# Kernel tuning notes

Hardware: AMD Instinct MI355X
Metric: run time of the kernel (lower is better)

Reference implementation:

```python
import jax, jax.numpy as jnp
import numpy as np

EPS = 1e-8
NUM_ITERATIONS = 3


def layer_norm(x, g, b, eps=EPS):
    m = jnp.mean(x, axis=-1, keepdims=True)
    v = jnp.mean((x - m) ** 2, axis=-1, keepdims=True)
    return (x - m) * jax.lax.rsqrt(v + eps) * g + b


def gru_cell(x, h, w_ih, w_hh, b_ih, b_hh):
    # PyTorch GRUCell: gates ordered (r, z, n)
    gi = x @ w_ih.T + b_ih  # [B*S, 3D]
    gh = h @ w_hh.T + b_hh
    i_r, i_z, i_n = jnp.split(gi, 3, axis=-1)
    h_r, h_z, h_n = jnp.split(gh, 3, axis=-1)
    r = jax.nn.sigmoid(i_r + h_r)
    z = jax.nn.sigmoid(i_z + h_z)
    n = jnp.tanh(i_n + r * h_n)
    return (1.0 - z) * n + z * h


def setup_inputs() -> dict:
    key = jax.random.key(0)
    ks = jax.random.split(key, 12)
    B, N, D, S = 64, 1024, 512, 16
    s = 1.0 / np.sqrt(D)
    return {
        "inputs": jax.random.normal(ks[0], (B, N, D), jnp.float32),
        "noise": jax.random.normal(ks[1], (B, S, D), jnp.float32),
        "slot_mu": jax.random.normal(ks[2], (1, 1, D), jnp.float32),
        "slot_log_sigma": jnp.zeros((1, 1, D), jnp.float32),
        "ln_in_g": jnp.ones((D,), jnp.float32),
        "ln_in_b": jnp.zeros((D,), jnp.float32),
        "ln_slots_g": jnp.ones((D,), jnp.float32),
        "ln_slots_b": jnp.zeros((D,), jnp.float32),
        "ln_mlp_g": jnp.ones((D,), jnp.float32),
        "ln_mlp_b": jnp.zeros((D,), jnp.float32),
        "Wq": jax.random.normal(ks[3], (D, D), jnp.float32) * s,
        "Wk": jax.random.normal(ks[4], (D, D), jnp.float32) * s,
        "Wv": jax.random.normal(ks[5], (D, D), jnp.float32) * s,
        "gru_w_ih": jax.random.normal(ks[6], (3 * D, D), jnp.float32) * s,
        "gru_w_hh": jax.random.normal(ks[7], (3 * D, D), jnp.float32) * s,
        "gru_b_ih": jnp.zeros((3 * D,), jnp.float32),
        "gru_b_hh": jnp.zeros((3 * D,), jnp.float32),
        "mlp_w1": jax.random.normal(ks[8], (D, D), jnp.float32) * s,
        "mlp_b1": jnp.zeros((D,), jnp.float32),
        "mlp_w2": jax.random.normal(ks[9], (D, D), jnp.float32) * s,
        "mlp_b2": jnp.zeros((D,), jnp.float32),
    }


def reference(inputs, noise, slot_mu, slot_log_sigma,
              ln_in_g, ln_in_b, ln_slots_g, ln_slots_b, ln_mlp_g, ln_mlp_b,
              Wq, Wk, Wv, gru_w_ih, gru_w_hh, gru_b_ih, gru_b_hh,
              mlp_w1, mlp_b1, mlp_w2, mlp_b2):
    B, N, D = inputs.shape
    S = noise.shape[1]
    scale = D ** (-0.5)

    # slot init: mu + sigma * eps
    slots = slot_mu + jnp.exp(slot_log_sigma) * noise  # [B,S,D]

    x = layer_norm(inputs, ln_in_g, ln_in_b)
    k = x @ Wk.T  # [B,N,D]
    v = x @ Wv.T

    for _ in range(NUM_ITERATIONS):
        slots_prev = slots
        sn = layer_norm(slots, ln_slots_g, ln_slots_b)
        q = sn @ Wq.T  # [B,S,D]
        attn_logits = jnp.einsum("bnd,bmd->bnm", q, k) * scale  # [B,S,N]
        attn = jax.nn.softmax(attn_logits, axis=-1)
        attn = attn / (jnp.sum(attn, axis=1, keepdims=True) + EPS)  # column-normalize over slots
        updates = jnp.einsum("bnm,bmd->bnd", attn, v)  # [B,S,D]
        slots = gru_cell(updates.reshape(-1, D), slots_prev.reshape(-1, D),
                         gru_w_ih, gru_w_hh, gru_b_ih, gru_b_hh).reshape(B, S, D)
        h = jax.nn.relu(layer_norm(slots, ln_mlp_g, ln_mlp_b) @ mlp_w1.T + mlp_b1)
        slots = slots + h @ mlp_w2.T + mlp_b2

    # proj_to_hidden is Identity (slot_dim == hidden_size); forward_dtype=float32
    return slots
```

## Files before the change

kernel.cpp:

```cpp
#include <hip/hip_runtime.h>
#include <hip/hip_bf16.h>
#include <cstdint>
#include <cstddef>


typedef __bf16 bf16x8 __attribute__((ext_vector_type(8)));
typedef float f32x4 __attribute__((ext_vector_type(4)));

__device__ __forceinline__ float bf2f(unsigned int u) {
  union { unsigned int i; float f; } v; v.i = u << 16; return v.f;
}
__device__ __forceinline__ unsigned short f2bf(float x) {
  __hip_bfloat16 h = __float2bfloat16(x);
  unsigned short u;
  __builtin_memcpy(&u, &h, 2);
  return u;
}

#define GLD16(gp, lp)                                                       \
  __builtin_amdgcn_global_load_lds(                                         \
      (const __attribute__((address_space(1))) void*)(gp),                  \
      (__attribute__((address_space(3))) void*)(lp), 16, 0, 0)


__global__ void wprep_k(const float* __restrict__ Wv, const float* __restrict__ w1,
                        const float* __restrict__ w2, const float* __restrict__ wih,
                        const float* __restrict__ whh, const float* __restrict__ bih,
                        const float* __restrict__ bhh, const float* __restrict__ mu,
                        const float* __restrict__ ls, const float* __restrict__ noise,
                        unsigned short* __restrict__ wv_bf, unsigned short* __restrict__ w1_bf,
                        unsigned short* __restrict__ w2_bf, unsigned short* __restrict__ wcat,
                        float* __restrict__ bcat, float* __restrict__ slots) {
  int blk = blockIdx.x, t = threadIdx.x;
  if (blk < 1024) {
    int i = blk * 256 + t; wv_bf[i] = f2bf(Wv[i]);
  } else if (blk < 2048) {
    int i = (blk - 1024) * 256 + t; w1_bf[i] = f2bf(w1[i]);
  } else if (blk < 3072) {
    int i = (blk - 2048) * 256 + t; w2_bf[i] = f2bf(w2[i]);
  } else if (blk < 11264) {
    int i = (blk - 3072) * 256 + t;
    int j = i >> 10, k = i & 1023;
    float v;
    if (j < 1024)      v = (k < 512) ? wih[j * 512 + k] : whh[j * 512 + (k - 512)];
    else if (j < 1536) v = (k < 512) ? wih[j * 512 + k] : 0.0f;
    else               v = (k < 512) ? 0.0f : whh[(j - 512) * 512 + (k - 512)];
    wcat[i] = f2bf(v);
  } else if (blk < 11272) {
    int j = (blk - 11264) * 256 + t;
    float v;
    if (j < 1024)      v = bih[j] + bhh[j];
    else if (j < 1536) v = bih[j];
    else               v = bhh[j - 512];
    bcat[j] = v;
  } else {
    int i = (blk - 11272) * 256 + t;
    int d = i & 511;
    slots[i] = mu[d] + expf(ls[d]) * noise[i];
  }
}

__global__ __launch_bounds__(256) void tcast2_k(const float* __restrict__ Wq,
                                                const float* __restrict__ Wk,
                                                unsigned short* __restrict__ wqT,
                                                unsigned short* __restrict__ wkT) {
  __shared__ float tt[32][33];
  const float* in = blockIdx.z ? Wk : Wq;
  unsigned short* out = blockIdx.z ? wkT : wqT;
  int c0 = blockIdx.x << 5, r0 = blockIdx.y << 5;
  int tx = threadIdx.x & 31, ty = threadIdx.x >> 5;
  #pragma unroll
  for (int i = 0; i < 4; ++i)
    tt[ty + 8 * i][tx] = in[(size_t)(r0 + ty + 8 * i) * 512 + c0 + tx];
  __syncthreads();
  #pragma unroll
  for (int i = 0; i < 4; ++i)
    out[(size_t)(c0 + ty + 8 * i) * 512 + r0 + tx] = f2bf(tt[tx][ty + 8 * i]);
}


__global__ __launch_bounds__(256) void ln_rows_k(
    const float* __restrict__ in, const float* __restrict__ g, const float* __restrict__ b,
    unsigned short* __restrict__ out, int rows) {
  int w = threadIdx.x >> 6, lane = threadIdx.x & 63;
  int row = (blockIdx.x << 2) + w;
  if (row >= rows) return;
  const float4* rp = reinterpret_cast<const float4*>(in + (size_t)row * 512);
  float4 v0 = rp[lane], v1 = rp[lane + 64];
  float s = v0.x + v0.y + v0.z + v0.w + v1.x + v1.y + v1.z + v1.w;
  float q = v0.x*v0.x + v0.y*v0.y + v0.z*v0.z + v0.w*v0.w
          + v1.x*v1.x + v1.y*v1.y + v1.z*v1.z + v1.w*v1.w;
  #pragma unroll
  for (int o = 32; o > 0; o >>= 1) { s += __shfl_xor(s, o); q += __shfl_xor(q, o); }
  float m = s * (1.0f / 512.0f);
  float rstd = rsqrtf(q * (1.0f / 512.0f) - m * m + 1e-8f);
  const float4* gp = reinterpret_cast<const float4*>(g);
  const float4* bp = reinterpret_cast<const float4*>(b);
  float4 g0 = gp[lane], g1 = gp[lane + 64];
  float4 b0 = bp[lane], b1 = bp[lane + 64];
  ushort4 o0, o1;
  o0.x = f2bf((v0.x - m) * rstd * g0.x + b0.x);
  o0.y = f2bf((v0.y - m) * rstd * g0.y + b0.y);
  o0.z = f2bf((v0.z - m) * rstd * g0.z + b0.z);
  o0.w = f2bf((v0.w - m) * rstd * g0.w + b0.w);
  o1.x = f2bf((v1.x - m) * rstd * g1.x + b1.x);
  o1.y = f2bf((v1.y - m) * rstd * g1.y + b1.y);
  o1.z = f2bf((v1.z - m) * rstd * g1.z + b1.z);
  o1.w = f2bf((v1.w - m) * rstd * g1.w + b1.w);
  ushort4* op = reinterpret_cast<ushort4*>(out + (size_t)row * 512);
  op[lane] = o0; op[lane + 64] = o1;
}

__global__ __launch_bounds__(256) void gru_ln_k(
    const float* __restrict__ gates, const float* __restrict__ hp,
    const float* __restrict__ g, const float* __restrict__ b,
    float* __restrict__ sgru, unsigned short* __restrict__ lnm) {
  int w = threadIdx.x >> 6, lane = threadIdx.x & 63;
  int row = (blockIdx.x << 2) + w;
  size_t gb = (size_t)row * 2048 + (lane << 3);
  size_t hb = (size_t)row * 512 + (lane << 3);
  float rs[8], zs[8], in_[8], hn[8], hv[8], y[8];
  #pragma unroll
  for (int c = 0; c < 2; ++c) {
    *reinterpret_cast<float4*>(rs + 4*c)  = *reinterpret_cast<const float4*>(gates + gb + 4*c);
    *reinterpret_cast<float4*>(zs + 4*c)  = *reinterpret_cast<const float4*>(gates + gb + 512 + 4*c);
    *reinterpret_cast<float4*>(in_ + 4*c) = *reinterpret_cast<const float4*>(gates + gb + 1024 + 4*c);
    *reinterpret_cast<float4*>(hn + 4*c)  = *reinterpret_cast<const float4*>(gates + gb + 1536 + 4*c);
    *reinterpret_cast<float4*>(hv + 4*c)  = *reinterpret_cast<const float4*>(hp + hb + 4*c);
  }
  float s = 0.f, q = 0.f;
  #pragma unroll
  for (int j = 0; j < 8; ++j) {
    float r = 1.0f / (1.0f + expf(-rs[j]));
    float z = 1.0f / (1.0f + expf(-zs[j]));
    float n = tanhf(in_[j] + r * hn[j]);
    float h = (1.0f - z) * n + z * hv[j];
    y[j] = h; s += h; q += h * h;
  }
  #pragma unroll
  for (int o = 32; o > 0; o >>= 1) { s += __shfl_xor(s, o); q += __shfl_xor(q, o); }
  float m = s * (1.0f / 512.0f);
  float rstd = rsqrtf(q * (1.0f / 512.0f) - m * m + 1e-8f);
  const float* gg = g + (lane << 3);
  const float* bb = b + (lane << 3);
  #pragma unroll
  for (int c = 0; c < 2; ++c)
    *reinterpret_cast<float4*>(sgru + hb + 4*c) = *reinterpret_cast<const float4*>(y + 4*c);
  uint4 o4;
  unsigned int p[8];
  #pragma unroll
  for (int j = 0; j < 8; ++j) p[j] = f2bf((y[j] - m) * rstd * gg[j] + bb[j]);
  o4.x = p[0] | (p[1] << 16); o4.y = p[2] | (p[3] << 16);
  o4.z = p[4] | (p[5] << 16); o4.w = p[6] | (p[7] << 16);
  *reinterpret_cast<uint4*>(lnm + hb) = o4;
}


__global__ __launch_bounds__(256) void gemm_vt(
    const unsigned short* __restrict__ A, const unsigned short* __restrict__ W,
    unsigned short* __restrict__ vT) {
  __shared__ unsigned short sA[2][4096];
  __shared__ unsigned short sB[2][4096];
  const int tid = threadIdx.x;
  const int lane = tid & 63, w = tid >> 6;

  int flat = blockIdx.y * 4 + blockIdx.x;
  { int c = 2048 >> 3; flat = (flat & 7) * c + (flat >> 3); }
  const int row0 = (flat >> 2) << 7;
  const int col0 = (flat & 3) << 7;
  const int K = 512;

  const int wm = (w >> 1) << 6, wn = (w & 1) << 6;
  const int lrow = lane & 15, kt = (lane >> 4) << 3;
  const int srow = lane >> 2, scol = (lane & 3) << 3;

  f32x4 acc[4][4];
  #pragma unroll
  for (int m = 0; m < 4; ++m)
    #pragma unroll
    for (int n = 0; n < 4; ++n) acc[m][n] = f32x4{0.f, 0.f, 0.f, 0.f};

  auto stage = [&](int buf, int k0) {
    #pragma unroll
    for (int i = 0; i < 2; ++i) {
      int ii = w * 2 + i;
      int r = (ii << 4) + srow;
      GLD16(A + (size_t)(row0 + r) * K + k0 + scol, &sA[buf][ii * 512]);
      GLD16(W + (size_t)(col0 + r) * K + k0 + scol, &sB[buf][ii * 512]);
    }
  };

  stage(0, 0);
  int cur = 0;
  for (int t = 0; t < 16; ++t) {
    __syncthreads();
    if (t + 1 < 16) stage(cur ^ 1, (t + 1) << 5);
    bf16x8 af[4], bfv[4];
    #pragma unroll
    for (int m = 0; m < 4; ++m)
      af[m] = *reinterpret_cast<const bf16x8*>(&sA[cur][(wm + m * 16 + lrow) * 32 + kt]);
    #pragma unroll
    for (int n = 0; n < 4; ++n)
      bfv[n] = *reinterpret_cast<const bf16x8*>(&sB[cur][(wn + n * 16 + lrow) * 32 + kt]);
    #pragma unroll
    for (int m = 0; m < 4; ++m)
      #pragma unroll
      for (int n = 0; n < 4; ++n)
        acc[m][n] = __builtin_amdgcn_mfma_f32_16x16x32_bf16(af[m], bfv[n], acc[m][n], 0, 0, 0);
    cur ^= 1;
  }

  const int rb = (lane >> 4) << 2;
  const int b = row0 >> 10;
  const int n0 = row0 & 1023;
  unsigned short* vb = vT + ((size_t)b << 19);
  #pragma unroll
  for (int m = 0; m < 4; ++m) {
    #pragma unroll
    for (int n = 0; n < 4; ++n) {
      int col = col0 + wn + n * 16 + lrow;
      int nn = n0 + wm + m * 16 + rb;
      ushort4 o;
      o.x = f2bf(acc[m][n][0]); o.y = f2bf(acc[m][n][1]);
      o.z = f2bf(acc[m][n][2]); o.w = f2bf(acc[m][n][3]);
      *reinterpret_cast<ushort4*>(vb + (size_t)col * 1024 + nn) = o;
    }
  }
}


__global__ __launch_bounds__(256) void q2ln_k(
    const float* __restrict__ slots, const float* __restrict__ g, const float* __restrict__ b,
    const unsigned short* __restrict__ wpt, unsigned short* __restrict__ q2,
    unsigned short* __restrict__ A2) {
  __shared__ unsigned short s_sn[16 * 520];
  __shared__ unsigned short sB[2][4096];
  const int b_ = blockIdx.y, ct = blockIdx.x;
  const int lane = threadIdx.x & 63, w = threadIdx.x >> 6;
  const int lrow = lane & 15, kt = (lane >> 4) << 3;
  const int srow = lane >> 2, scol = (lane & 3) << 3;

  const float4* gp = reinterpret_cast<const float4*>(g);
  const float4* bp = reinterpret_cast<const float4*>(b);
  float4 g0 = gp[lane], g1 = gp[lane + 64];
  float4 b0 = bp[lane], b1 = bp[lane + 64];
  #pragma unroll
  for (int rr = 0; rr < 4; ++rr) {
    int r = w * 4 + rr;
    const float4* rp = reinterpret_cast<const float4*>(slots + (size_t)(b_ * 16 + r) * 512);
    float4 v0 = rp[lane], v1 = rp[lane + 64];
    float s = v0.x + v0.y + v0.z + v0.w + v1.x + v1.y + v1.z + v1.w;
    float q = v0.x*v0.x + v0.y*v0.y + v0.z*v0.z + v0.w*v0.w
            + v1.x*v1.x + v1.y*v1.y + v1.z*v1.z + v1.w*v1.w;
    #pragma unroll
    for (int o = 32; o > 0; o >>= 1) { s += __shfl_xor(s, o); q += __shfl_xor(q, o); }
    float m = s * (1.0f / 512.0f);
    float rstd = rsqrtf(q * (1.0f / 512.0f) - m * m + 1e-8f);
    ushort4 o0, o1;
    o0.x = f2bf((v0.x - m) * rstd * g0.x + b0.x);
    o0.y = f2bf((v0.y - m) * rstd * g0.y + b0.y);
    o0.z = f2bf((v0.z - m) * rstd * g0.z + b0.z);
    o0.w = f2bf((v0.w - m) * rstd * g0.w + b0.w);
    o1.x = f2bf((v1.x - m) * rstd * g1.x + b1.x);
    o1.y = f2bf((v1.y - m) * rstd * g1.y + b1.y);
    o1.z = f2bf((v1.z - m) * rstd * g1.z + b1.z);
    o1.w = f2bf((v1.w - m) * rstd * g1.w + b1.w);
    *reinterpret_cast<ushort4*>(&s_sn[r * 520 + lane * 4]) = o0;
    *reinterpret_cast<ushort4*>(&s_sn[r * 520 + 256 + lane * 4]) = o1;
    if (ct == 0) {
      ushort4 c0, c1;
      c0.x = f2bf(v0.x); c0.y = f2bf(v0.y); c0.z = f2bf(v0.z); c0.w = f2bf(v0.w);
      c1.x = f2bf(v1.x); c1.y = f2bf(v1.y); c1.z = f2bf(v1.z); c1.w = f2bf(v1.w);
      unsigned short* a2r = A2 + (size_t)(b_ * 16 + r) * 1024 + 512;
      *reinterpret_cast<ushort4*>(a2r + lane * 4) = c0;
      *reinterpret_cast<ushort4*>(a2r + 256 + lane * 4) = c1;
    }
  }

  const unsigned short* Bb = wpt + (size_t)(ct << 7) * 512;
  auto stage = [&](int buf, int k0) {
    #pragma unroll
    for (int i = 0; i < 2; ++i) {
      int ii = w * 2 + i;
      GLD16(Bb + (size_t)((ii << 4) + srow) * 512 + k0 + scol, &sB[buf][ii * 512]);
    }
  };

  f32x4 acc[2];
  acc[0] = f32x4{0.f, 0.f, 0.f, 0.f};
  acc[1] = f32x4{0.f, 0.f, 0.f, 0.f};

  stage(0, 0);
  int cur = 0;
  for (int t = 0; t < 16; ++t) {
    __syncthreads();
    if (t + 1 < 16) stage(cur ^ 1, (t + 1) << 5);
    bf16x8 af = *reinterpret_cast<const bf16x8*>(&s_sn[lrow * 520 + (t << 5) + kt]);
    #pragma unroll
    for (int ni = 0; ni < 2; ++ni) {
      bf16x8 bfv = *reinterpret_cast<const bf16x8*>(&sB[cur][((w * 2 + ni) * 16 + lrow) * 32 + kt]);
      acc[ni] = __builtin_amdgcn_mfma_f32_16x16x32_bf16(af, bfv, acc[ni], 0, 0, 0);
    }
    cur ^= 1;
  }

  const int rb = (lane >> 4) << 2;
  #pragma unroll
  for (int ni = 0; ni < 2; ++ni) {
    int col = (ct << 7) + (w * 2 + ni) * 16 + lrow;
    #pragma unroll
    for (int r = 0; r < 4; ++r) {
      int s = rb + r;
      q2[(size_t)((b_ << 4) + s) * 512 + col] = f2bf(acc[ni][r]);
    }
  }
}


__global__ __launch_bounds__(256) void logits_k(
    const unsigned short* __restrict__ q2, const unsigned short* __restrict__ x,
    float* __restrict__ out) {
  __shared__ unsigned short sA[2][512];
  __shared__ unsigned short sB[2][4096];
  const int b = blockIdx.y, nt = blockIdx.x;
  const int lane = threadIdx.x & 63, w = threadIdx.x >> 6;
  const int lrow = lane & 15, kt = (lane >> 4) << 3;
  const int srow = lane >> 2, scol = (lane & 3) << 3;
  const unsigned short* Ab = q2 + ((size_t)b << 13);
  const unsigned short* Bb = x + (((size_t)(b << 10) + (nt << 7)) << 9);

  f32x4 acc[2];
  acc[0] = f32x4{0.f, 0.f, 0.f, 0.f};
  acc[1] = f32x4{0.f, 0.f, 0.f, 0.f};

  auto stage = [&](int buf, int k0) {
    #pragma unroll
    for (int i = 0; i < 2; ++i) {
      int ii = w * 2 + i;
      GLD16(Bb + (size_t)((ii << 4) + srow) * 512 + k0 + scol, &sB[buf][ii * 512]);
    }
    if (w == 0)
      GLD16(Ab + (size_t)srow * 512 + k0 + scol, &sA[buf][0]);
  };

  stage(0, 0);
  int cur = 0;
  for (int t = 0; t < 16; ++t) {
    __syncthreads();
    if (t + 1 < 16) stage(cur ^ 1, (t + 1) << 5);
    bf16x8 af = *reinterpret_cast<const bf16x8*>(&sA[cur][lrow * 32 + kt]);
    #pragma unroll
    for (int ni = 0; ni < 2; ++ni) {
      bf16x8 bfv = *reinterpret_cast<const bf16x8*>(&sB[cur][((w * 2 + ni) * 16 + lrow) * 32 + kt]);
      acc[ni] = __builtin_amdgcn_mfma_f32_16x16x32_bf16(af, bfv, acc[ni], 0, 0, 0);
    }
    cur ^= 1;
  }

  const int rb = (lane >> 4) << 2;
  #pragma unroll
  for (int ni = 0; ni < 2; ++ni) {
    int n = (nt << 7) + (w * 2 + ni) * 16 + lrow;
    #pragma unroll
    for (int r = 0; r < 4; ++r) {
      int s = rb + r;
      out[(size_t)((b << 4) + s) * 1024 + n] = acc[ni][r];
    }
  }
}


__global__ __launch_bounds__(256) void pv_sm_k(
    const float* __restrict__ logits, const unsigned short* __restrict__ vT,
    unsigned short* __restrict__ A2) {
  __shared__ float s_mi[16][2];
  __shared__ unsigned short s_at[16 * 1032];
  __shared__ unsigned short sA[2][4096];
  const int b_ = blockIdx.y, dt = blockIdx.x;
  const int lane = threadIdx.x & 63, w = threadIdx.x >> 6;
  const int lrow = lane & 15, kt = (lane >> 4) << 3;
  const int srow = lane >> 2, scol = (lane & 3) << 3;
  const float* lg = logits + ((size_t)b_ << 14);

  #pragma unroll
  for (int rr = 0; rr < 4; ++rr) {
    int r = w * 4 + rr;
    const float* rp = lg + (size_t)r * 1024;
    float v[16];
    float mx = -3.4e38f;
    #pragma unroll
    for (int i = 0; i < 16; ++i) { v[i] = rp[lane + (i << 6)]; mx = fmaxf(mx, v[i]); }
    #pragma unroll
    for (int o = 32; o > 0; o >>= 1) mx = fmaxf(mx, __shfl_xor(mx, o));
    float s = 0.f;
    #pragma unroll
    for (int i = 0; i < 16; ++i) s += __expf(v[i] - mx);
    #pragma unroll
    for (int o = 32; o > 0; o >>= 1) s += __shfl_xor(s, o);
    if (lane == 0) { s_mi[r][0] = mx; s_mi[r][1] = 1.0f / s; }
  }
  __syncthreads();

  #pragma unroll
  for (int j = 0; j < 4; ++j) {
    int c = threadIdx.x + (j << 8);
    float e[16];
    float cs = 0.f;
    #pragma unroll
    for (int s = 0; s < 16; ++s) {
      e[s] = __expf(lg[(size_t)s * 1024 + c] - s_mi[s][0]) * s_mi[s][1];
      cs += e[s];
    }
    float rv = 1.0f / (cs + 1e-8f);
    #pragma unroll
    for (int s = 0; s < 16; ++s) s_at[s * 1032 + c] = f2bf(e[s] * rv);
  }

  const unsigned short* Ab = vT + ((size_t)b_ << 19) + (size_t)(dt << 7) * 1024;
  auto stage = [&](int buf, int k0) {
    #pragma unroll
    for (int i = 0; i < 2; ++i) {
      int ii = w * 2 + i;
      GLD16(Ab + (size_t)((ii << 4) + srow) * 1024 + k0 + scol, &sA[buf][ii * 512]);
    }
  };

  f32x4 acc[2];
  acc[0] = f32x4{0.f, 0.f, 0.f, 0.f};
  acc[1] = f32x4{0.f, 0.f, 0.f, 0.f};

  stage(0, 0);
  int cur = 0;
  for (int t = 0; t < 32; ++t) {
    __syncthreads();
    if (t + 1 < 32) stage(cur ^ 1, (t + 1) << 5);
    bf16x8 bfv = *reinterpret_cast<const bf16x8*>(&s_at[lrow * 1032 + (t << 5) + kt]);
    #pragma unroll
    for (int mi = 0; mi < 2; ++mi) {
      bf16x8 af = *reinterpret_cast<const bf16x8*>(&sA[cur][((w * 2 + mi) * 16 + lrow) * 32 + kt]);
      acc[mi] = __builtin_amdgcn_mfma_f32_16x16x32_bf16(af, bfv, acc[mi], 0, 0, 0);
    }
    cur ^= 1;
  }

  const int rb = (lane >> 4) << 2;
  const int s = lrow;
  #pragma unroll
  for (int mi = 0; mi < 2; ++mi) {
    int d0 = (dt << 7) + (w * 2 + mi) * 16 + rb;
    ushort4 o;
    o.x = f2bf(acc[mi][0]); o.y = f2bf(acc[mi][1]);
    o.z = f2bf(acc[mi][2]); o.w = f2bf(acc[mi][3]);
    *reinterpret_cast<ushort4*>(&A2[(size_t)((b_ << 4) + s) * 1024 + d0]) = o;
  }
}


template<int BIAS, int RELU, int ADDSRC, int OUTBF16, int SCALE>
__global__ __launch_bounds__(256) void gemm_sm(
    const unsigned short* __restrict__ A, const unsigned short* __restrict__ W,
    const float* __restrict__ bias, const float* __restrict__ addsrc,
    void* __restrict__ Cout, int M, int N, int K, float scalev) {
  __shared__ unsigned short sA[2][2048];
  __shared__ unsigned short sB[2][2048];
  const int tid = threadIdx.x;
  const int lane = tid & 63, w = tid >> 6;

  int nwg = gridDim.x * gridDim.y;
  int flat = blockIdx.y * gridDim.x + blockIdx.x;
  if ((nwg & 7) == 0) { int c = nwg >> 3; flat = (flat & 7) * c + (flat >> 3); }
  const int row0 = (flat / gridDim.x) << 6;
  const int col0 = (flat % gridDim.x) << 6;

  const int lrow = lane & 15, kt = (lane >> 4) << 3;
  const int srow = lane >> 2, scol = (lane & 3) << 3;

  f32x4 acc[4];
  #pragma unroll
  for (int m = 0; m < 4; ++m) acc[m] = f32x4{0.f, 0.f, 0.f, 0.f};

  auto stage = [&](int buf, int k0) {
    int r = (w << 4) + srow;
    GLD16(A + (size_t)(row0 + r) * K + k0 + scol, &sA[buf][w * 512]);
    GLD16(W + (size_t)(col0 + r) * K + k0 + scol, &sB[buf][w * 512]);
  };

  stage(0, 0);
  const int nt = K >> 5;
  int cur = 0;
  for (int t = 0; t < nt; ++t) {
    __syncthreads();
    if (t + 1 < nt) stage(cur ^ 1, (t + 1) << 5);
    bf16x8 af[4], bfv;
    #pragma unroll
    for (int m = 0; m < 4; ++m)
      af[m] = *reinterpret_cast<const bf16x8*>(&sA[cur][(m * 16 + lrow) * 32 + kt]);
    bfv = *reinterpret_cast<const bf16x8*>(&sB[cur][((w << 4) + lrow) * 32 + kt]);
    #pragma unroll
    for (int m = 0; m < 4; ++m)
      acc[m] = __builtin_amdgcn_mfma_f32_16x16x32_bf16(af[m], bfv, acc[m], 0, 0, 0);
    cur ^= 1;
  }

  const int rb = (lane >> 4) << 2;
  const int col = col0 + (w << 4) + lrow;
  float bv = BIAS ? bias[col] : 0.0f;
  #pragma unroll
  for (int m = 0; m < 4; ++m) {
    #pragma unroll
    for (int r = 0; r < 4; ++r) {
      int row = row0 + m * 16 + rb + r;
      float v = acc[m][r];
      if (SCALE) v *= scalev;
      v += bv;
      if (ADDSRC) v += addsrc[(size_t)row * N + col];
      if (RELU) v = fmaxf(v, 0.0f);
      if (OUTBF16) ((unsigned short*)Cout)[(size_t)row * N + col] = f2bf(v);
      else ((float*)Cout)[(size_t)row * N + col] = v;
    }
  }
}


extern "C" void kernel_launch(void* const* d_in, const int* in_sizes, int n_in,
                              void* d_out, int out_size, void* d_ws, size_t ws_size,
                              hipStream_t stream) {
  const float* inputs  = (const float*)d_in[0];
  const float* noise   = (const float*)d_in[1];
  const float* slot_mu = (const float*)d_in[2];
  const float* slot_ls = (const float*)d_in[3];
  const float* ln_in_g = (const float*)d_in[4];
  const float* ln_in_b = (const float*)d_in[5];
  const float* ln_s_g  = (const float*)d_in[6];
  const float* ln_s_b  = (const float*)d_in[7];
  const float* ln_m_g  = (const float*)d_in[8];
  const float* ln_m_b  = (const float*)d_in[9];
  const float* Wq   = (const float*)d_in[10];
  const float* Wk   = (const float*)d_in[11];
  const float* Wv   = (const float*)d_in[12];
  const float* w_ih = (const float*)d_in[13];
  const float* w_hh = (const float*)d_in[14];
  const float* b_ih = (const float*)d_in[15];
  const float* b_hh = (const float*)d_in[16];
  const float* w1   = (const float*)d_in[17];
  const float* b1   = (const float*)d_in[18];
  const float* w2   = (const float*)d_in[19];
  const float* b2   = (const float*)d_in[20];

  const int BN = 65536, BS = 1024;

  uintptr_t base = (uintptr_t)d_ws;
  auto alloc = [&](size_t bytes) {
    void* p = (void*)base;
    base += (bytes + 255) & ~(size_t)255;
    return p;
  };
  unsigned short* x_bf    = (unsigned short*)alloc((size_t)BN * 512 * 2);
  unsigned short* vT      = (unsigned short*)alloc((size_t)64 * 512 * 1024 * 2);
  unsigned short* wqT     = (unsigned short*)alloc(512 * 512 * 2);
  unsigned short* wkT     = (unsigned short*)alloc(512 * 512 * 2);
  unsigned short* wpt     = (unsigned short*)alloc(512 * 512 * 2);
  unsigned short* wv_bf   = (unsigned short*)alloc(512 * 512 * 2);
  unsigned short* wcat_bf = (unsigned short*)alloc((size_t)2048 * 1024 * 2);
  float*          bcat    = (float*)alloc(2048 * 4);
  unsigned short* w1_bf   = (unsigned short*)alloc(512 * 512 * 2);
  unsigned short* w2_bf   = (unsigned short*)alloc(512 * 512 * 2);
  float*          slots   = (float*)alloc((size_t)BS * 512 * 4);
  unsigned short* A2      = (unsigned short*)alloc((size_t)BS * 1024 * 2);
  unsigned short* q2_bf   = (unsigned short*)alloc((size_t)BS * 512 * 2);
  float*          logits  = (float*)alloc((size_t)64 * 16 * 1024 * 4);
  float*          gates   = (float*)alloc((size_t)BS * 2048 * 4);
  float*          sgru    = (float*)alloc((size_t)BS * 512 * 4);
  unsigned short* lnm_bf  = (unsigned short*)alloc((size_t)BS * 512 * 2);
  unsigned short* h_bf    = (unsigned short*)alloc((size_t)BS * 512 * 2);
  (void)ws_size; (void)n_in; (void)in_sizes; (void)out_size;

  const float scale = 0.044194173824159216f;

  wprep_k<<<13320, 256, 0, stream>>>(Wv, w1, w2, w_ih, w_hh, b_ih, b_hh,
                                     slot_mu, slot_ls, noise,
                                     wv_bf, w1_bf, w2_bf, wcat_bf, bcat, slots);
  tcast2_k<<<dim3(16, 16, 2), 256, 0, stream>>>(Wq, Wk, wqT, wkT);
  gemm_sm<0,0,0,1,1><<<dim3(8, 8), 256, 0, stream>>>(
      wkT, wqT, nullptr, nullptr, wpt, 512, 512, 512, scale);
  ln_rows_k<<<16384, 256, 0, stream>>>(inputs, ln_in_g, ln_in_b, x_bf, BN);
  gemm_vt<<<dim3(4, 512), 256, 0, stream>>>(x_bf, wv_bf, vT);

  for (int it = 0; it < 3; ++it) {
    q2ln_k<<<dim3(4, 64), 256, 0, stream>>>(slots, ln_s_g, ln_s_b, wpt, q2_bf, A2);
    logits_k<<<dim3(8, 64), 256, 0, stream>>>(q2_bf, x_bf, logits);
    pv_sm_k<<<dim3(4, 64), 256, 0, stream>>>(logits, vT, A2);
    gemm_sm<1,0,0,0,0><<<dim3(32, 16), 256, 0, stream>>>(
        A2, wcat_bf, bcat, nullptr, gates, BS, 2048, 1024, 1.0f);
    gru_ln_k<<<256, 256, 0, stream>>>(gates, slots, ln_m_g, ln_m_b, sgru, lnm_bf);
    gemm_sm<1,1,0,1,0><<<dim3(8, 16), 256, 0, stream>>>(
        lnm_bf, w1_bf, b1, nullptr, h_bf, BS, 512, 512, 1.0f);
    float* slots_out = (it == 2) ? (float*)d_out : slots;
    gemm_sm<1,0,1,0,0><<<dim3(8, 16), 256, 0, stream>>>(
        h_bf, w2_bf, b2, sgru, slots_out, BS, 512, 512, 1.0f);
  }
}
```

Before: 368.9 us.

## Use 128x128-tile GEMM for slot GEMMs and store logits in bf16

Adds a gemm_bt kernel with 128x128 output tiles, each wave computing a 4x4 grid of MFMA fragments. It replaces the 64x64 gemm_sm for the GRU gate, MLP1 and MLP2 GEMMs to get more reuse per staged tile. The attention logits buffer now holds bf16 instead of fp32, halving the bytes written by logits_k and read by pv_sm_k, at some cost in softmax input precision. Grids become much smaller (128 and 32 workgroups), which may leave many CUs idle on these small-M GEMMs.

```diff
diff --git a/kernel.cpp b/kernel.cpp
--- a/kernel.cpp
+++ b/kernel.cpp
@@ -156,6 +156,84 @@
 }
 
 
+template<int BIAS, int RELU, int ADDSRC, int OUTBF16>
+__global__ __launch_bounds__(256) void gemm_bt(
+    const unsigned short* __restrict__ A, const unsigned short* __restrict__ W,
+    const float* __restrict__ bias, const float* __restrict__ addsrc,
+    void* __restrict__ Cout, int M, int N, int K) {
+  __shared__ unsigned short sA[2][4096];
+  __shared__ unsigned short sB[2][4096];
+  const int tid = threadIdx.x;
+  const int lane = tid & 63, w = tid >> 6;
+
+  int nwg = gridDim.x * gridDim.y;
+  int flat = blockIdx.y * gridDim.x + blockIdx.x;
+  if ((nwg & 7) == 0) { int c = nwg >> 3; flat = (flat & 7) * c + (flat >> 3); }
+  const int row0 = (flat / gridDim.x) << 7;
+  const int col0 = (flat % gridDim.x) << 7;
+
+  const int wm = (w >> 1) << 6, wn = (w & 1) << 6;
+  const int lrow = lane & 15, kt = (lane >> 4) << 3;
+  const int srow = lane >> 2, scol = (lane & 3) << 3;
+
+  f32x4 acc[4][4];
+  #pragma unroll
+  for (int m = 0; m < 4; ++m)
+    #pragma unroll
+    for (int n = 0; n < 4; ++n) acc[m][n] = f32x4{0.f, 0.f, 0.f, 0.f};
+
+  auto stage = [&](int buf, int k0) {
+    #pragma unroll
+    for (int i = 0; i < 2; ++i) {
+      int ii = w * 2 + i;
+      int r = (ii << 4) + srow;
+      GLD16(A + (size_t)(row0 + r) * K + k0 + scol, &sA[buf][ii * 512]);
+      GLD16(W + (size_t)(col0 + r) * K + k0 + scol, &sB[buf][ii * 512]);
+    }
+  };
+
+  stage(0, 0);
+  const int nt = K >> 5;
+  int cur = 0;
+  for (int t = 0; t < nt; ++t) {
+    __syncthreads();
+    if (t + 1 < nt) stage(cur ^ 1, (t + 1) << 5);
+    bf16x8 af[4], bfv[4];
+    #pragma unroll
+    for (int m = 0; m < 4; ++m)
+      af[m] = *reinterpret_cast<const bf16x8*>(&sA[cur][(wm + m * 16 + lrow) * 32 + kt]);
+    #pragma unroll
+    for (int n = 0; n < 4; ++n)
+      bfv[n] = *reinterpret_cast<const bf16x8*>(&sB[cur][(wn + n * 16 + lrow) * 32 + kt]);
+    #pragma unroll
+    for (int m = 0; m < 4; ++m)
+      #pragma unroll
+      for (int n = 0; n < 4; ++n)
+        acc[m][n] = __builtin_amdgcn_mfma_f32_16x16x32_bf16(af[m], bfv[n], acc[m][n], 0, 0, 0);
+    cur ^= 1;
+  }
+
+  const int rb = (lane >> 4) << 2;
+  #pragma unroll
+  for (int m = 0; m < 4; ++m) {
+    #pragma unroll
+    for (int n = 0; n < 4; ++n) {
+      int col = col0 + wn + n * 16 + lrow;
+      float bv = BIAS ? bias[col] : 0.0f;
+      #pragma unroll
+      for (int r = 0; r < 4; ++r) {
+        int row = row0 + wm + m * 16 + rb + r;
+        float v = acc[m][n][r] + bv;
+        if (ADDSRC) v += addsrc[(size_t)row * N + col];
+        if (RELU) v = fmaxf(v, 0.0f);
+        if (OUTBF16) ((unsigned short*)Cout)[(size_t)row * N + col] = f2bf(v);
+        else ((float*)Cout)[(size_t)row * N + col] = v;
+      }
+    }
+  }
+}
+
+
 __global__ __launch_bounds__(256) void gemm_vt(
     const unsigned short* __restrict__ A, const unsigned short* __restrict__ W,
     unsigned short* __restrict__ vT) {
@@ -319,7 +397,7 @@
 
 __global__ __launch_bounds__(256) void logits_k(
     const unsigned short* __restrict__ q2, const unsigned short* __restrict__ x,
-    float* __restrict__ out) {
+    unsigned short* __restrict__ out) {
   __shared__ unsigned short sA[2][512];
   __shared__ unsigned short sB[2][4096];
   const int b = blockIdx.y, nt = blockIdx.x;
@@ -364,14 +442,14 @@
     #pragma unroll
     for (int r = 0; r < 4; ++r) {
       int s = rb + r;
-      out[(size_t)((b << 4) + s) * 1024 + n] = acc[ni][r];
+      out[(size_t)((b << 4) + s) * 1024 + n] = f2bf(acc[ni][r]);
     }
   }
 }
 
 
 __global__ __launch_bounds__(256) void pv_sm_k(
-    const float* __restrict__ logits, const unsigned short* __restrict__ vT,
+    const unsigned short* __restrict__ logits, const unsigned short* __restrict__ vT,
     unsigned short* __restrict__ A2) {
   __shared__ float s_mi[16][2];
   __shared__ unsigned short s_at[16 * 1032];
@@ -380,16 +458,16 @@
   const int lane = threadIdx.x & 63, w = threadIdx.x >> 6;
   const int lrow = lane & 15, kt = (lane >> 4) << 3;
   const int srow = lane >> 2, scol = (lane & 3) << 3;
-  const float* lg = logits + ((size_t)b_ << 14);
+  const unsigned short* lg = logits + ((size_t)b_ << 14);
 
   #pragma unroll
   for (int rr = 0; rr < 4; ++rr) {
     int r = w * 4 + rr;
-    const float* rp = lg + (size_t)r * 1024;
+    const unsigned short* rp = lg + (size_t)r * 1024;
     float v[16];
     float mx = -3.4e38f;
     #pragma unroll
-    for (int i = 0; i < 16; ++i) { v[i] = rp[lane + (i << 6)]; mx = fmaxf(mx, v[i]); }
+    for (int i = 0; i < 16; ++i) { v[i] = bf2f(rp[lane + (i << 6)]); mx = fmaxf(mx, v[i]); }
     #pragma unroll
     for (int o = 32; o > 0; o >>= 1) mx = fmaxf(mx, __shfl_xor(mx, o));
     float s = 0.f;
@@ -408,7 +486,7 @@
     float cs = 0.f;
     #pragma unroll
     for (int s = 0; s < 16; ++s) {
-      e[s] = __expf(lg[(size_t)s * 1024 + c] - s_mi[s][0]) * s_mi[s][1];
+      e[s] = __expf(bf2f(lg[(size_t)s * 1024 + c]) - s_mi[s][0]) * s_mi[s][1];
       cs += e[s];
     }
     float rv = 1.0f / (cs + 1e-8f);
@@ -456,10 +534,9 @@
 }
 
 
-template<int BIAS, int RELU, int ADDSRC, int OUTBF16, int SCALE>
+template<int OUTBF16, int SCALE>
 __global__ __launch_bounds__(256) void gemm_sm(
     const unsigned short* __restrict__ A, const unsigned short* __restrict__ W,
-    const float* __restrict__ bias, const float* __restrict__ addsrc,
     void* __restrict__ Cout, int M, int N, int K, float scalev) {
   __shared__ unsigned short sA[2][2048];
   __shared__ unsigned short sB[2][2048];
@@ -504,7 +581,6 @@
 
   const int rb = (lane >> 4) << 2;
   const int col = col0 + (w << 4) + lrow;
-  float bv = BIAS ? bias[col] : 0.0f;
   #pragma unroll
   for (int m = 0; m < 4; ++m) {
     #pragma unroll
@@ -512,9 +588,6 @@
       int row = row0 + m * 16 + rb + r;
       float v = acc[m][r];
       if (SCALE) v *= scalev;
-      v += bv;
-      if (ADDSRC) v += addsrc[(size_t)row * N + col];
-      if (RELU) v = fmaxf(v, 0.0f);
       if (OUTBF16) ((unsigned short*)Cout)[(size_t)row * N + col] = f2bf(v);
       else ((float*)Cout)[(size_t)row * N + col] = v;
     }
@@ -568,7 +641,7 @@
   float*          slots   = (float*)alloc((size_t)BS * 512 * 4);
   unsigned short* A2      = (unsigned short*)alloc((size_t)BS * 1024 * 2);
   unsigned short* q2_bf   = (unsigned short*)alloc((size_t)BS * 512 * 2);
-  float*          logits  = (float*)alloc((size_t)64 * 16 * 1024 * 4);
+  unsigned short* logits  = (unsigned short*)alloc((size_t)64 * 16 * 1024 * 2);
   float*          gates   = (float*)alloc((size_t)BS * 2048 * 4);
   float*          sgru    = (float*)alloc((size_t)BS * 512 * 4);
   unsigned short* lnm_bf  = (unsigned short*)alloc((size_t)BS * 512 * 2);
@@ -581,8 +654,8 @@
                                      slot_mu, slot_ls, noise,
                                      wv_bf, w1_bf, w2_bf, wcat_bf, bcat, slots);
   tcast2_k<<<dim3(16, 16, 2), 256, 0, stream>>>(Wq, Wk, wqT, wkT);
-  gemm_sm<0,0,0,1,1><<<dim3(8, 8), 256, 0, stream>>>(
-      wkT, wqT, nullptr, nullptr, wpt, 512, 512, 512, scale);
+  gemm_sm<1,1><<<dim3(8, 8), 256, 0, stream>>>(
+      wkT, wqT, wpt, 512, 512, 512, scale);
   ln_rows_k<<<16384, 256, 0, stream>>>(inputs, ln_in_g, ln_in_b, x_bf, BN);
   gemm_vt<<<dim3(4, 512), 256, 0, stream>>>(x_bf, wv_bf, vT);
 
@@ -590,13 +663,13 @@
     q2ln_k<<<dim3(4, 64), 256, 0, stream>>>(slots, ln_s_g, ln_s_b, wpt, q2_bf, A2);
     logits_k<<<dim3(8, 64), 256, 0, stream>>>(q2_bf, x_bf, logits);
     pv_sm_k<<<dim3(4, 64), 256, 0, stream>>>(logits, vT, A2);
-    gemm_sm<1,0,0,0,0><<<dim3(32, 16), 256, 0, stream>>>(
-        A2, wcat_bf, bcat, nullptr, gates, BS, 2048, 1024, 1.0f);
+    gemm_bt<1,0,0,0><<<dim3(16, 8), 256, 0, stream>>>(
+        A2, wcat_bf, bcat, nullptr, gates, BS, 2048, 1024);
     gru_ln_k<<<256, 256, 0, stream>>>(gates, slots, ln_m_g, ln_m_b, sgru, lnm_bf);
-    gemm_sm<1,1,0,1,0><<<dim3(8, 16), 256, 0, stream>>>(
-        lnm_bf, w1_bf, b1, nullptr, h_bf, BS, 512, 512, 1.0f);
+    gemm_bt<1,1,0,1><<<dim3(4, 8), 256, 0, stream>>>(
+        lnm_bf, w1_bf, b1, nullptr, h_bf, BS, 512, 512);
     float* slots_out = (it == 2) ? (float*)d_out : slots;
-    gemm_sm<1,0,1,0,0><<<dim3(8, 16), 256, 0, stream>>>(
-        h_bf, w2_bf, b2, sgru, slots_out, BS, 512, 512, 1.0f);
-  }
-}
+    gemm_bt<1,0,1,0><<<dim3(4, 8), 256, 0, stream>>>(
+        h_bf, w2_bf, b2, sgru, slots_out, BS, 512, 512);
+  }
+}
```

Measured after the change: 406.0 us. 1.1x slower.

## Fold Wv into GRU input weights and attend over transposed normalized inputs

Applied to the files above, without the earlier changes.

Stops computing V = x·Wv^T for all 65536 input rows. Instead it precomputes W_ih·Wv once and folds it into the concatenated GRU weight, so attention-weighted sums run directly over a transposed bf16 copy of the normalized inputs. This replaces a large GEMM with a cheap transpose, though the transposed copy still has to be written. Attention logits are also stored as bf16 instead of fp32, which halves that traffic but adds rounding error before the softmax.

```diff
diff --git a/kernel.cpp b/kernel.cpp
--- a/kernel.cpp
+++ b/kernel.cpp
@@ -23,50 +23,54 @@
       (__attribute__((address_space(3))) void*)(lp), 16, 0, 0)
 
 
-__global__ void wprep_k(const float* __restrict__ Wv, const float* __restrict__ w1,
-                        const float* __restrict__ w2, const float* __restrict__ wih,
-                        const float* __restrict__ whh, const float* __restrict__ bih,
+__global__ void wprep_k(const float* __restrict__ w1, const float* __restrict__ w2,
+                        const float* __restrict__ wih, const float* __restrict__ bih,
                         const float* __restrict__ bhh, const float* __restrict__ mu,
                         const float* __restrict__ ls, const float* __restrict__ noise,
-                        unsigned short* __restrict__ wv_bf, unsigned short* __restrict__ w1_bf,
-                        unsigned short* __restrict__ w2_bf, unsigned short* __restrict__ wcat,
-                        float* __restrict__ bcat, float* __restrict__ slots) {
+                        unsigned short* __restrict__ w1_bf, unsigned short* __restrict__ w2_bf,
+                        unsigned short* __restrict__ wih_bf, float* __restrict__ bcat,
+                        float* __restrict__ slots) {
   int blk = blockIdx.x, t = threadIdx.x;
   if (blk < 1024) {
-    int i = blk * 256 + t; wv_bf[i] = f2bf(Wv[i]);
+    int i = blk * 256 + t; w1_bf[i] = f2bf(w1[i]);
   } else if (blk < 2048) {
-    int i = (blk - 1024) * 256 + t; w1_bf[i] = f2bf(w1[i]);
-  } else if (blk < 3072) {
-    int i = (blk - 2048) * 256 + t; w2_bf[i] = f2bf(w2[i]);
-  } else if (blk < 11264) {
-    int i = (blk - 3072) * 256 + t;
-    int j = i >> 10, k = i & 1023;
-    float v;
-    if (j < 1024)      v = (k < 512) ? wih[j * 512 + k] : whh[j * 512 + (k - 512)];
-    else if (j < 1536) v = (k < 512) ? wih[j * 512 + k] : 0.0f;
-    else               v = (k < 512) ? 0.0f : whh[(j - 512) * 512 + (k - 512)];
-    wcat[i] = f2bf(v);
-  } else if (blk < 11272) {
-    int j = (blk - 11264) * 256 + t;
+    int i = (blk - 1024) * 256 + t; w2_bf[i] = f2bf(w2[i]);
+  } else if (blk < 5120) {
+    int i = (blk - 2048) * 256 + t; wih_bf[i] = f2bf(wih[i]);
+  } else if (blk < 5128) {
+    int j = (blk - 5120) * 256 + t;
     float v;
     if (j < 1024)      v = bih[j] + bhh[j];
     else if (j < 1536) v = bih[j];
     else               v = bhh[j - 512];
     bcat[j] = v;
   } else {
-    int i = (blk - 11272) * 256 + t;
+    int i = (blk - 5128) * 256 + t;
     int d = i & 511;
     slots[i] = mu[d] + expf(ls[d]) * noise[i];
   }
 }
 
-__global__ __launch_bounds__(256) void tcast2_k(const float* __restrict__ Wq,
+__global__ void wcat_k(const float* __restrict__ wihp, const float* __restrict__ whh,
+                       unsigned short* __restrict__ out) {
+  int i = blockIdx.x * 256 + threadIdx.x;
+  int j = i >> 10, k = i & 1023;
+  float v;
+  if (j < 1024)      v = (k < 512) ? wihp[j * 512 + k] : whh[j * 512 + (k - 512)];
+  else if (j < 1536) v = (k < 512) ? wihp[j * 512 + k] : 0.0f;
+  else               v = (k < 512) ? 0.0f : whh[(j - 512) * 512 + (k - 512)];
+  out[i] = f2bf(v);
+}
+
+__global__ __launch_bounds__(256) void tcast3_k(const float* __restrict__ Wq,
                                                 const float* __restrict__ Wk,
+                                                const float* __restrict__ Wv,
                                                 unsigned short* __restrict__ wqT,
-                                                unsigned short* __restrict__ wkT) {
+                                                unsigned short* __restrict__ wkT,
+                                                unsigned short* __restrict__ wvT) {
   __shared__ float tt[32][33];
-  const float* in = blockIdx.z ? Wk : Wq;
-  unsigned short* out = blockIdx.z ? wkT : wqT;
+  const float* in = blockIdx.z == 0 ? Wq : (blockIdx.z == 1 ? Wk : Wv);
+  unsigned short* out = blockIdx.z == 0 ? wqT : (blockIdx.z == 1 ? wkT : wvT);
   int c0 = blockIdx.x << 5, r0 = blockIdx.y << 5;
   int tx = threadIdx.x & 31, ty = threadIdx.x >> 5;
   #pragma unroll
@@ -111,6 +115,33 @@
   op[lane] = o0; op[lane + 64] = o1;
 }
 
+
+__global__ __launch_bounds__(256) void xt_k(const unsigned short* __restrict__ x,
+                                            unsigned short* __restrict__ xT) {
+  __shared__ unsigned short t[64][68];
+  int nt = blockIdx.x, et = blockIdx.y, b = blockIdx.z;
+  int r = threadIdx.x >> 3, c8 = (threadIdx.x & 7) << 3;
+  #pragma unroll
+  for (int p = 0; p < 2; ++p) {
+    int row = r + (p << 5);
+    *reinterpret_cast<uint4*>(&t[row][c8]) = *reinterpret_cast<const uint4*>(
+        x + ((size_t)(b << 10) + (nt << 6) + row) * 512 + (et << 6) + c8);
+  }
+  __syncthreads();
+  #pragma unroll
+  for (int p = 0; p < 2; ++p) {
+    int erow = r + (p << 5);
+    ushort4 a, bb;
+    #pragma unroll
+    for (int j = 0; j < 4; ++j) ((unsigned short*)&a)[j] = t[c8 + j][erow];
+    #pragma unroll
+    for (int j = 0; j < 4; ++j) ((unsigned short*)&bb)[j] = t[c8 + 4 + j][erow];
+    unsigned short* o = xT + ((size_t)(b << 9) + (et << 6) + erow) * 1024 + (nt << 6) + c8;
+    *reinterpret_cast<ushort4*>(o) = a;
+    *reinterpret_cast<ushort4*>(o + 4) = bb;
+  }
+}
+
 __global__ __launch_bounds__(256) void gru_ln_k(
     const float* __restrict__ gates, const float* __restrict__ hp,
     const float* __restrict__ g, const float* __restrict__ b,
@@ -156,19 +187,20 @@
 }
 
 
-__global__ __launch_bounds__(256) void gemm_vt(
+template<int OUTBF16>
+__global__ __launch_bounds__(256) void gemm_bt(
     const unsigned short* __restrict__ A, const unsigned short* __restrict__ W,
-    unsigned short* __restrict__ vT) {
+    void* __restrict__ Cout, int M, int N, int K) {
   __shared__ unsigned short sA[2][4096];
   __shared__ unsigned short sB[2][4096];
   const int tid = threadIdx.x;
   const int lane = tid & 63, w = tid >> 6;
 
-  int flat = blockIdx.y * 4 + blockIdx.x;
-  { int c = 2048 >> 3; flat = (flat & 7) * c + (flat >> 3); }
-  const int row0 = (flat >> 2) << 7;
-  const int col0 = (flat & 3) << 7;
-  const int K = 512;
+  int nwg = gridDim.x * gridDim.y;
+  int flat = blockIdx.y * gridDim.x + blockIdx.x;
+  if ((nwg & 7) == 0) { int c = nwg >> 3; flat = (flat & 7) * c + (flat >> 3); }
+  const int row0 = (flat / gridDim.x) << 7;
+  const int col0 = (flat % gridDim.x) << 7;
 
   const int wm = (w >> 1) << 6, wn = (w & 1) << 6;
   const int lrow = lane & 15, kt = (lane >> 4) << 3;
@@ -191,10 +223,11 @@
   };
 
   stage(0, 0);
+  const int nt = K >> 5;
   int cur = 0;
-  for (int t = 0; t < 16; ++t) {
+  for (int t = 0; t < nt; ++t) {
     __syncthreads();
-    if (t + 1 < 16) stage(cur ^ 1, (t + 1) << 5);
+    if (t + 1 < nt) stage(cur ^ 1, (t + 1) << 5);
     bf16x8 af[4], bfv[4];
     #pragma unroll
     for (int m = 0; m < 4; ++m)
@@ -211,19 +244,18 @@
   }
 
   const int rb = (lane >> 4) << 2;
-  const int b = row0 >> 10;
-  const int n0 = row0 & 1023;
-  unsigned short* vb = vT + ((size_t)b << 19);
   #pragma unroll
   for (int m = 0; m < 4; ++m) {
     #pragma unroll
     for (int n = 0; n < 4; ++n) {
       int col = col0 + wn + n * 16 + lrow;
-      int nn = n0 + wm + m * 16 + rb;
-      ushort4 o;
-      o.x = f2bf(acc[m][n][0]); o.y = f2bf(acc[m][n][1]);
-      o.z = f2bf(acc[m][n][2]); o.w = f2bf(acc[m][n][3]);
-      *reinterpret_cast<ushort4*>(vb + (size_t)col * 1024 + nn) = o;
+      #pragma unroll
+      for (int r = 0; r < 4; ++r) {
+        int row = row0 + wm + m * 16 + rb + r;
+        float v = acc[m][n][r];
+        if (OUTBF16) ((unsigned short*)Cout)[(size_t)row * N + col] = f2bf(v);
+        else ((float*)Cout)[(size_t)row * N + col] = v;
+      }
     }
   }
 }
@@ -319,7 +351,7 @@
 
 __global__ __launch_bounds__(256) void logits_k(
     const unsigned short* __restrict__ q2, const unsigned short* __restrict__ x,
-    float* __restrict__ out) {
+    unsigned short* __restrict__ out) {
   __shared__ unsigned short sA[2][512];
   __shared__ unsigned short sB[2][4096];
   const int b = blockIdx.y, nt = blockIdx.x;
@@ -364,32 +396,32 @@
     #pragma unroll
     for (int r = 0; r < 4; ++r) {
       int s = rb + r;
-      out[(size_t)((b << 4) + s) * 1024 + n] = acc[ni][r];
+      out[(size_t)((b << 4) + s) * 1024 + n] = f2bf(acc[ni][r]);
     }
   }
 }
 
 
 __global__ __launch_bounds__(256) void pv_sm_k(
-    const float* __restrict__ logits, const unsigned short* __restrict__ vT,
+    const unsigned short* __restrict__ logits, const unsigned short* __restrict__ xT,
     unsigned short* __restrict__ A2) {
   __shared__ float s_mi[16][2];
   __shared__ unsigned short s_at[16 * 1032];
   __shared__ unsigned short sA[2][4096];
-  const int b_ = blockIdx.y, dt = blockIdx.x;
+  const int b_ = blockIdx.y, et = blockIdx.x;
   const int lane = threadIdx.x & 63, w = threadIdx.x >> 6;
   const int lrow = lane & 15, kt = (lane >> 4) << 3;
   const int srow = lane >> 2, scol = (lane & 3) << 3;
-  const float* lg = logits + ((size_t)b_ << 14);
+  const unsigned short* lg = logits + ((size_t)b_ << 14);
 
   #pragma unroll
   for (int rr = 0; rr < 4; ++rr) {
     int r = w * 4 + rr;
-    const float* rp = lg + (size_t)r * 1024;
+    const unsigned short* rp = lg + (size_t)r * 1024;
     float v[16];
     float mx = -3.4e38f;
     #pragma unroll
-    for (int i = 0; i < 16; ++i) { v[i] = rp[lane + (i << 6)]; mx = fmaxf(mx, v[i]); }
+    for (int i = 0; i < 16; ++i) { v[i] = bf2f(rp[lane + (i << 6)]); mx = fmaxf(mx, v[i]); }
     #pragma unroll
     for (int o = 32; o > 0; o >>= 1) mx = fmaxf(mx, __shfl_xor(mx, o));
     float s = 0.f;
@@ -408,7 +440,7 @@
     float cs = 0.f;
     #pragma unroll
     for (int s = 0; s < 16; ++s) {
-      e[s] = __expf(lg[(size_t)s * 1024 + c] - s_mi[s][0]) * s_mi[s][1];
+      e[s] = __expf(bf2f(lg[(size_t)s * 1024 + c]) - s_mi[s][0]) * s_mi[s][1];
       cs += e[s];
     }
     float rv = 1.0f / (cs + 1e-8f);
@@ -416,7 +448,7 @@
     for (int s = 0; s < 16; ++s) s_at[s * 1032 + c] = f2bf(e[s] * rv);
   }
 
-  const unsigned short* Ab = vT + ((size_t)b_ << 19) + (size_t)(dt << 7) * 1024;
+  const unsigned short* Ab = xT + ((size_t)b_ << 19) + (size_t)(et << 7) * 1024;
   auto stage = [&](int buf, int k0) {
     #pragma unroll
     for (int i = 0; i < 2; ++i) {
@@ -447,11 +479,11 @@
   const int s = lrow;
   #pragma unroll
   for (int mi = 0; mi < 2; ++mi) {
-    int d0 = (dt << 7) + (w * 2 + mi) * 16 + rb;
+    int e0 = (et << 7) + (w * 2 + mi) * 16 + rb;
     ushort4 o;
     o.x = f2bf(acc[mi][0]); o.y = f2bf(acc[mi][1]);
     o.z = f2bf(acc[mi][2]); o.w = f2bf(acc[mi][3]);
-    *reinterpret_cast<ushort4*>(&A2[(size_t)((b_ << 4) + s) * 1024 + d0]) = o;
+    *reinterpret_cast<ushort4*>(&A2[(size_t)((b_ << 4) + s) * 1024 + e0]) = o;
   }
 }
 
@@ -556,11 +588,13 @@
     return p;
   };
   unsigned short* x_bf    = (unsigned short*)alloc((size_t)BN * 512 * 2);
-  unsigned short* vT      = (unsigned short*)alloc((size_t)64 * 512 * 1024 * 2);
+  unsigned short* xT      = (unsigned short*)alloc((size_t)64 * 512 * 1024 * 2);
   unsigned short* wqT     = (unsigned short*)alloc(512 * 512 * 2);
   unsigned short* wkT     = (unsigned short*)alloc(512 * 512 * 2);
+  unsigned short* wvT     = (unsigned short*)alloc(512 * 512 * 2);
   unsigned short* wpt     = (unsigned short*)alloc(512 * 512 * 2);
-  unsigned short* wv_bf   = (unsigned short*)alloc(512 * 512 * 2);
+  unsigned short* wih_bf  = (unsigned short*)alloc((size_t)1536 * 512 * 2);
+  float*          wihp    = (float*)alloc((size_t)1536 * 512 * 4);
   unsigned short* wcat_bf = (unsigned short*)alloc((size_t)2048 * 1024 * 2);
   float*          bcat    = (float*)alloc(2048 * 4);
   unsigned short* w1_bf   = (unsigned short*)alloc(512 * 512 * 2);
@@ -568,7 +602,7 @@
   float*          slots   = (float*)alloc((size_t)BS * 512 * 4);
   unsigned short* A2      = (unsigned short*)alloc((size_t)BS * 1024 * 2);
   unsigned short* q2_bf   = (unsigned short*)alloc((size_t)BS * 512 * 2);
-  float*          logits  = (float*)alloc((size_t)64 * 16 * 1024 * 4);
+  unsigned short* logits  = (unsigned short*)alloc((size_t)64 * 16 * 1024 * 2);
   float*          gates   = (float*)alloc((size_t)BS * 2048 * 4);
   float*          sgru    = (float*)alloc((size_t)BS * 512 * 4);
   unsigned short* lnm_bf  = (unsigned short*)alloc((size_t)BS * 512 * 2);
@@ -577,19 +611,21 @@
 
   const float scale = 0.044194173824159216f;
 
-  wprep_k<<<13320, 256, 0, stream>>>(Wv, w1, w2, w_ih, w_hh, b_ih, b_hh,
-                                     slot_mu, slot_ls, noise,
-                                     wv_bf, w1_bf, w2_bf, wcat_bf, bcat, slots);
-  tcast2_k<<<dim3(16, 16, 2), 256, 0, stream>>>(Wq, Wk, wqT, wkT);
+  wprep_k<<<7176, 256, 0, stream>>>(w1, w2, w_ih, b_ih, b_hh, slot_mu, slot_ls, noise,
+                                    w1_bf, w2_bf, wih_bf, bcat, slots);
+  tcast3_k<<<dim3(16, 16, 3), 256, 0, stream>>>(Wq, Wk, Wv, wqT, wkT, wvT);
   gemm_sm<0,0,0,1,1><<<dim3(8, 8), 256, 0, stream>>>(
       wkT, wqT, nullptr, nullptr, wpt, 512, 512, 512, scale);
+  gemm_bt<0><<<dim3(4, 12), 256, 0, stream>>>(
+      wih_bf, wvT, wihp, 1536, 512, 512);
+  wcat_k<<<8192, 256, 0, stream>>>(wihp, w_hh, wcat_bf);
   ln_rows_k<<<16384, 256, 0, stream>>>(inputs, ln_in_g, ln_in_b, x_bf, BN);
-  gemm_vt<<<dim3(4, 512), 256, 0, stream>>>(x_bf, wv_bf, vT);
+  xt_k<<<dim3(16, 8, 64), 256, 0, stream>>>(x_bf, xT);
 
   for (int it = 0; it < 3; ++it) {
     q2ln_k<<<dim3(4, 64), 256, 0, stream>>>(slots, ln_s_g, ln_s_b, wpt, q2_bf, A2);
     logits_k<<<dim3(8, 64), 256, 0, stream>>>(q2_bf, x_bf, logits);
-    pv_sm_k<<<dim3(4, 64), 256, 0, stream>>>(logits, vT, A2);
+    pv_sm_k<<<dim3(4, 64), 256, 0, stream>>>(logits, xT, A2);
     gemm_sm<1,0,0,0,0><<<dim3(32, 16), 256, 0, stream>>>(
         A2, wcat_bf, bcat, nullptr, gates, BS, 2048, 1024, 1.0f);
     gru_ln_k<<<256, 256, 0, stream>>>(gates, slots, ln_m_g, ln_m_b, sgru, lnm_bf);
```

After: 344.0 us. 6.8% less time.
